# Performance work log

Measured on AMD Instinct MI355X. Metric: run time of the kernel, lower is better.

Reference implementation:

```python
import jax, jax.numpy as jnp
import numpy as np

N = 1024   # state dimension
L = 16384  # sequence length


def setup_inputs() -> dict:
    key = jax.random.key(0)
    k_u, k_a, k_b, k_c = jax.random.split(key, 4)
    u = jax.random.normal(k_u, (L,), dtype=jnp.float32)
    # lecun_normal: std = 1/sqrt(fan_in). Shift A by -I so the discretized
    # transition matrix Ab has spectral radius < 1 (otherwise Ab^L overflows).
    A = jax.random.normal(k_a, (N, N), dtype=jnp.float32) / np.sqrt(N) - jnp.eye(N, dtype=jnp.float32)
    B = jax.random.normal(k_b, (N, 1), dtype=jnp.float32) / np.sqrt(1.0)
    C = jax.random.normal(k_c, (1, N), dtype=jnp.float32) / np.sqrt(N)
    log_step = jnp.full((1, 1), np.log(0.01), dtype=jnp.float32)
    return {"u": u, "A": A, "B": B, "C": C, "log_step": log_step}


def reference(u, A, B, C, log_step):
    # --- discretize (bilinear / Tustin transform) ---
    step = jnp.exp(log_step)[0, 0]
    I = jnp.eye(A.shape[0], dtype=A.dtype)
    BL = jnp.linalg.inv(I - (step / 2.0) * A)
    Ab = BL @ (I + (step / 2.0) * A)     # (N, N)
    Bb = (step * BL) @ B                  # (N, 1)
    Cb = C                                # (1, N)

    # --- naive_kernel: K[l] = Cb @ Ab^l @ Bb, built as a scan recurrence ---
    def body(x, _):
        k_l = (Cb @ x)[0, 0]
        return Ab @ x, k_l

    _, K = jax.lax.scan(body, Bb, None, length=u.shape[0])  # (L,)

    # --- causal convolution: y[t] = sum_{l<=t} K[l] * u[t-l] ---
    y = jnp.convolve(u, K)[: u.shape[0]]
    return y
```

## Files before the change

### kernel.cpp

```cpp
#include <hip/hip_runtime.h>
#include <hip/hip_bf16.h>
#include <math.h>

#define N_DIM 1024
#define L_SEQ 16384

typedef unsigned short ushort_t;
typedef __bf16 bf16x8 __attribute__((ext_vector_type(8)));
typedef float f32x4 __attribute__((ext_vector_type(4)));

#define FW_F32 1
#define FW_SPLIT 2
#define FW_TSPLIT 4
#define FW_ADDD 8
#define FW_MKAB 16
#define FW_TPRE 32

#define AS1 __attribute__((address_space(1)))
#define AS3 __attribute__((address_space(3)))

__device__ __forceinline__ void split2(float v, ushort_t& h, ushort_t& m) {
  union { __bf16 b; ushort_t u; } c;
  __bf16 bh = (__bf16)v;
  float fh = (float)bh;
  c.b = bh; h = c.u;
  c.b = (__bf16)(v - fh); m = c.u;
}

__global__ __launch_bounds__(256) void k_scalesplit(const float* __restrict__ A,
    const float* __restrict__ ls, float* __restrict__ E,
    ushort_t* __restrict__ set) {
  const size_t NN = (size_t)N_DIM * N_DIM;
  float hs = 0.5f * expf(ls[0]);
  int t = threadIdx.x;
  int r0 = blockIdx.x * 64 + ((t >> 4) << 2);
  int c0 = blockIdx.y * 64 + ((t & 15) << 2);
  float v[4][4];
#pragma unroll
  for (int i = 0; i < 4; ++i) {
    float4 f = *(const float4*)&A[(size_t)(r0 + i) * N_DIM + c0];
    v[i][0] = hs * f.x; v[i][1] = hs * f.y; v[i][2] = hs * f.z; v[i][3] = hs * f.w;
    *(float4*)&E[(size_t)(r0 + i) * N_DIM + c0] =
        make_float4(v[i][0], v[i][1], v[i][2], v[i][3]);
  }
  ushort_t h[4][4], m[4][4];
#pragma unroll
  for (int i = 0; i < 4; ++i)
#pragma unroll
    for (int j = 0; j < 4; ++j) split2(v[i][j], h[i][j], m[i][j]);
#pragma unroll
  for (int i = 0; i < 4; ++i) {
    size_t o = (size_t)(r0 + i) * N_DIM + c0;
    *(ushort4*)&set[o] = make_ushort4(h[i][0], h[i][1], h[i][2], h[i][3]);
    *(ushort4*)&set[NN + o] = make_ushort4(m[i][0], m[i][1], m[i][2], m[i][3]);
  }
#pragma unroll
  for (int j = 0; j < 4; ++j) {
    size_t o = (size_t)(c0 + j) * N_DIM + r0;
    *(ushort4*)&set[2 * NN + o] = make_ushort4(h[0][j], h[1][j], h[2][j], h[3][j]);
    *(ushort4*)&set[3 * NN + o] = make_ushort4(m[0][j], m[1][j], m[2][j], m[3][j]);
  }
}

__global__ __launch_bounds__(256) void k_bbinit(ushort_t* __restrict__ VTset,
    ushort_t* __restrict__ Wset, const float* __restrict__ S,
    const float* __restrict__ B, const float* __restrict__ Cm,
    const float* __restrict__ ls) {
  const size_t KR = (size_t)128 * N_DIM;
  int bx = blockIdx.x;
  if (bx >= 256) {
    int i = (bx - 256) * 256 + threadIdx.x;
    ushort_t h, m; split2(Cm[i], h, m);
    Wset[i] = h; Wset[KR + i] = m;
    return;
  }
  int row = bx * 4 + (threadIdx.x >> 6);
  int lane = threadIdx.x & 63;
  const float* Sr = S + (size_t)row * N_DIM;
  float sum = 0.f;
  for (int k = lane; k < N_DIM; k += 64) sum += Sr[k] * B[k];
  for (int off = 32; off; off >>= 1) sum += __shfl_down(sum, off);
  if (lane == 0) {
    float step = expf(ls[0]);
    float bb = step * (B[row] + sum);
    ushort_t h, m; split2(bb, h, m);
    VTset[row] = h; VTset[KR + row] = m;
  }
}

__global__ __launch_bounds__(256) void gemm4f(
    const ushort_t* __restrict__ Qa, const ushort_t* __restrict__ Qbt,
    const float* __restrict__ D, float* __restrict__ Cf,
    ushort_t* __restrict__ Oset, ushort_t* __restrict__ Oset2, int flags,
    const ushort_t* __restrict__ SkB, ushort_t* __restrict__ Ka,
    int srcOff, int dstOff, int cnt, int mode) {
  const size_t NN = (size_t)N_DIM * N_DIM;
  const size_t KR = (size_t)128 * N_DIM;
  __shared__ __align__(16) ushort_t lds[32768];
  int t = threadIdx.x;
  const int lane = t & 63, w = t >> 6;
  bool isSk = (mode == 2) || (mode == 1 && (int)blockIdx.y >= 16);

  if (!isSk) {
    int m0 = blockIdx.x * 64, n0 = blockIdx.y * 64;
    int r = t & 63, kc = t >> 6;
    const ushort_t* gA[2] = {Qa, Qa + NN};
    const ushort_t* gB[2] = {Qbt, Qbt + NN};
    size_t aoff = (size_t)(m0 + r) * N_DIM + kc * 8;
    size_t boff = (size_t)(n0 + r) * N_DIM + kc * 8;

    auto stage = [&](int buf, int k0) {
      ushort_t* dst = lds + buf * 8192;
#pragma unroll
      for (int L = 0; L < 2; ++L) {
        __builtin_amdgcn_global_load_lds(
            (const AS1 void*)(gA[L] + aoff + k0),
            (AS3 void*)(dst + L * 2048 + t * 8), 16, 0, 0);
        __builtin_amdgcn_global_load_lds(
            (const AS1 void*)(gB[L] + boff + k0),
            (AS3 void*)(dst + 4096 + L * 2048 + t * 8), 16, 0, 0);
      }
    };

    f32x4 acc[2][2];
#pragma unroll
    for (int i = 0; i < 2; ++i)
#pragma unroll
      for (int j = 0; j < 2; ++j) acc[i][j] = (f32x4){0.f, 0.f, 0.f, 0.f};

    const int wm = (w >> 1) * 32, wn = (w & 1) * 32;
    const int lrow = lane & 15, kg = lane >> 4;
    const int aIdx0 = kg * 512 + (wm + lrow) * 8;
    const int bIdx0 = 4096 + kg * 512 + (wn + lrow) * 8;

    stage(0, 0);
    stage(1, 32);
    stage(2, 64);
    for (int ks = 0; ks < 32; ++ks) {
      int cur = ks & 3;
      if (ks < 29) {
        stage((ks + 3) & 3, (ks + 3) * 32);
        asm volatile("s_waitcnt vmcnt(12)" ::: "memory");
      } else if (ks == 29) {
        asm volatile("s_waitcnt vmcnt(8)" ::: "memory");
      } else if (ks == 30) {
        asm volatile("s_waitcnt vmcnt(4)" ::: "memory");
      } else {
        asm volatile("s_waitcnt vmcnt(0)" ::: "memory");
      }
      __builtin_amdgcn_s_barrier();
      __builtin_amdgcn_sched_barrier(0);
      const ushort_t* buf = lds + cur * 8192;
      bf16x8 a[2][2], b[2][2];
#pragma unroll
      for (int L = 0; L < 2; ++L) {
#pragma unroll
        for (int mi = 0; mi < 2; ++mi)
          a[L][mi] = *(const bf16x8*)&buf[L * 2048 + aIdx0 + mi * 128];
#pragma unroll
        for (int ni = 0; ni < 2; ++ni)
          b[L][ni] = *(const bf16x8*)&buf[bIdx0 + L * 2048 + ni * 128];
      }
#pragma unroll
      for (int mi = 0; mi < 2; ++mi)
#pragma unroll
        for (int ni = 0; ni < 2; ++ni) {
          f32x4 c = acc[mi][ni];
          c = __builtin_amdgcn_mfma_f32_16x16x32_bf16(a[0][mi], b[0][ni], c, 0, 0, 0);
          c = __builtin_amdgcn_mfma_f32_16x16x32_bf16(a[0][mi], b[1][ni], c, 0, 0, 0);
          c = __builtin_amdgcn_mfma_f32_16x16x32_bf16(a[1][mi], b[0][ni], c, 0, 0, 0);
          c = __builtin_amdgcn_mfma_f32_16x16x32_bf16(a[1][mi], b[1][ni], c, 0, 0, 0);
          acc[mi][ni] = c;
        }
      if (ks < 31) __builtin_amdgcn_s_barrier();
    }

#pragma unroll
    for (int mi = 0; mi < 2; ++mi)
#pragma unroll
      for (int ni = 0; ni < 2; ++ni) {
        int rowb = m0 + wm + mi * 16 + kg * 4;
        int col = n0 + wn + ni * 16 + lrow;
        float vv[4];
#pragma unroll
        for (int j = 0; j < 4; ++j) vv[j] = acc[mi][ni][j];
        if (flags & FW_TPRE) {
          ushort_t h[4], m[4];
#pragma unroll
          for (int j = 0; j < 4; ++j) split2(vv[j], h[j], m[j]);
          size_t o = (size_t)col * N_DIM + rowb;
          *(ushort4*)&Oset2[2 * NN + o] = make_ushort4(h[0], h[1], h[2], h[3]);
          *(ushort4*)&Oset2[3 * NN + o] = make_ushort4(m[0], m[1], m[2], m[3]);
        }
        if (flags & FW_ADDD) {
#pragma unroll
          for (int j = 0; j < 4; ++j) vv[j] += D[(size_t)(rowb + j) * N_DIM + col];
        }
        if (flags & FW_F32) {
#pragma unroll
          for (int j = 0; j < 4; ++j) Cf[(size_t)(rowb + j) * N_DIM + col] = vv[j];
        }
        if (flags & FW_MKAB) {
#pragma unroll
          for (int j = 0; j < 4; ++j)
            vv[j] = 2.0f * vv[j] + ((rowb + j) == col ? 1.0f : 0.0f);
        }
        if (flags & (FW_SPLIT | FW_TSPLIT)) {
          ushort_t h[4], m[4];
#pragma unroll
          for (int j = 0; j < 4; ++j) split2(vv[j], h[j], m[j]);
          if (flags & FW_SPLIT) {
#pragma unroll
            for (int j = 0; j < 4; ++j) {
              size_t o = (size_t)(rowb + j) * N_DIM + col;
              Oset[o] = h[j]; Oset[NN + o] = m[j];
            }
          }
          if (flags & FW_TSPLIT) {
            size_t o = (size_t)col * N_DIM + rowb;
            *(ushort4*)&Oset[2 * NN + o] = make_ushort4(h[0], h[1], h[2], h[3]);
            *(ushort4*)&Oset[3 * NN + o] = make_ushort4(m[0], m[1], m[2], m[3]);
          }
        }
      }
    return;
  }

  int id = (mode == 1) ? ((int)blockIdx.y - 16) * 16 + (int)blockIdx.x
                       : (int)blockIdx.y * 16 + (int)blockIdx.x;
  int rt = id >> 4, ct = id & 15;
  if (rt >= ((cnt + 15) >> 4)) return;
  const ushort_t* Ah = Ka;
  const ushort_t* Amm = Ka + KR;
  const ushort_t* Bh = SkB;
  const ushort_t* Bm = SkB + NN;
  const int lrow = lane & 15, kg = lane >> 4;

  auto stageS = [&](int buf, int k0) {
    ushort_t* base = lds + buf * 5120;
    if (t < 128) {
      int lvl = t >> 6, rem = t & 63, kcc = rem >> 4, i = rem & 15;
      const ushort_t* src = (lvl ? Amm : Ah) +
          (size_t)(srcOff + rt * 16 + i) * N_DIM + k0 + kcc * 8;
      __builtin_amdgcn_global_load_lds((const AS1 void*)src,
                                       (AS3 void*)(base + t * 8), 16, 0, 0);
    }
#pragma unroll
    for (int it2 = 0; it2 < 2; ++it2) {
      int t2 = t + it2 * 256;
      int lvl = t2 >> 8, rem = t2 & 255, kcc = rem >> 6, c = rem & 63;
      const ushort_t* src =
          (lvl ? Bm : Bh) + (size_t)(ct * 64 + c) * N_DIM + k0 + kcc * 8;
      __builtin_amdgcn_global_load_lds(
          (const AS1 void*)src, (AS3 void*)(base + 1024 + t2 * 8), 16, 0, 0);
    }
  };

  f32x4 acc = (f32x4){0.f, 0.f, 0.f, 0.f};
  const int aO = kg * 128 + lrow * 8;
  const int bO = 1024 + kg * 512 + (w * 16 + lrow) * 8;

  stageS(0, 0);
  stageS(1, 32);
  for (int ks2 = 0; ks2 < 32; ++ks2) {
    int cur = ks2 % 3;
    if (ks2 < 30) {
      stageS((ks2 + 2) % 3, (ks2 + 2) * 32);
      if (w < 2) asm volatile("s_waitcnt vmcnt(6)" ::: "memory");
      else       asm volatile("s_waitcnt vmcnt(4)" ::: "memory");
    } else if (ks2 == 30) {
      if (w < 2) asm volatile("s_waitcnt vmcnt(3)" ::: "memory");
      else       asm volatile("s_waitcnt vmcnt(2)" ::: "memory");
    } else {
      asm volatile("s_waitcnt vmcnt(0)" ::: "memory");
    }
    __builtin_amdgcn_s_barrier();
    __builtin_amdgcn_sched_barrier(0);
    const ushort_t* b = lds + cur * 5120;
    bf16x8 a0 = *(const bf16x8*)&b[aO];
    bf16x8 a1 = *(const bf16x8*)&b[aO + 512];
    bf16x8 b0v = *(const bf16x8*)&b[bO];
    bf16x8 b1v = *(const bf16x8*)&b[bO + 2048];
    acc = __builtin_amdgcn_mfma_f32_16x16x32_bf16(a0, b0v, acc, 0, 0, 0);
    acc = __builtin_amdgcn_mfma_f32_16x16x32_bf16(a0, b1v, acc, 0, 0, 0);
    acc = __builtin_amdgcn_mfma_f32_16x16x32_bf16(a1, b0v, acc, 0, 0, 0);
    acc = __builtin_amdgcn_mfma_f32_16x16x32_bf16(a1, b1v, acc, 0, 0, 0);
    if (ks2 < 31) __builtin_amdgcn_s_barrier();
  }

  int col = ct * 64 + w * 16 + lrow;
#pragma unroll
  for (int j = 0; j < 4; ++j) {
    int ir = rt * 16 + kg * 4 + j;
    if (ir < cnt) {
      ushort_t h, m; split2(acc[j], h, m);
      Ka[(size_t)(dstOff + ir) * N_DIM + col] = h;
      Ka[KR + (size_t)(dstOff + ir) * N_DIM + col] = m;
    }
  }
}

__global__ __launch_bounds__(256) void k_combine(
    const ushort_t* __restrict__ Wset, const ushort_t* __restrict__ Vset,
    float* __restrict__ Kv) {
  const size_t KR = (size_t)128 * N_DIM;
  __shared__ __align__(16) ushort_t lds[15360];
  int t = threadIdx.x;
  int rt = blockIdx.x, ct = blockIdx.y;
  const ushort_t* Ah = Wset;
  const ushort_t* Amm = Wset + KR;
  const ushort_t* Bh = Vset;
  const ushort_t* Bm = Vset + KR;
  const int lane = t & 63, w = t >> 6;
  const int lrow = lane & 15, kg = lane >> 4;

  auto stageS = [&](int buf, int k0) {
    ushort_t* base = lds + buf * 5120;
    if (t < 128) {
      int lvl = t >> 6, rem = t & 63, kcc = rem >> 4, i = rem & 15;
      const ushort_t* src =
          (lvl ? Amm : Ah) + (size_t)(rt * 16 + i) * N_DIM + k0 + kcc * 8;
      __builtin_amdgcn_global_load_lds((const AS1 void*)src,
                                       (AS3 void*)(base + t * 8), 16, 0, 0);
    }
#pragma unroll
    for (int it = 0; it < 2; ++it) {
      int t2 = t + it * 256;
      int lvl = t2 >> 8, rem = t2 & 255, kcc = rem >> 6, c = rem & 63;
      const ushort_t* src =
          (lvl ? Bm : Bh) + (size_t)(ct * 64 + c) * N_DIM + k0 + kcc * 8;
      __builtin_amdgcn_global_load_lds(
          (const AS1 void*)src, (AS3 void*)(base + 1024 + t2 * 8), 16, 0, 0);
    }
  };

  f32x4 acc = (f32x4){0.f, 0.f, 0.f, 0.f};
  const int aO = kg * 128 + lrow * 8;
  const int bO = 1024 + kg * 512 + (w * 16 + lrow) * 8;

  stageS(0, 0);
  stageS(1, 32);
  for (int ks = 0; ks < 32; ++ks) {
    int cur = ks % 3;
    if (ks < 30) {
      stageS((ks + 2) % 3, (ks + 2) * 32);
      if (w < 2) asm volatile("s_waitcnt vmcnt(6)" ::: "memory");
      else       asm volatile("s_waitcnt vmcnt(4)" ::: "memory");
    } else if (ks == 30) {
      if (w < 2) asm volatile("s_waitcnt vmcnt(3)" ::: "memory");
      else       asm volatile("s_waitcnt vmcnt(2)" ::: "memory");
    } else {
      asm volatile("s_waitcnt vmcnt(0)" ::: "memory");
    }
    __builtin_amdgcn_s_barrier();
    __builtin_amdgcn_sched_barrier(0);
    const ushort_t* b = lds + cur * 5120;
    bf16x8 a0 = *(const bf16x8*)&b[aO];
    bf16x8 a1 = *(const bf16x8*)&b[aO + 512];
    bf16x8 b0v = *(const bf16x8*)&b[bO];
    bf16x8 b1v = *(const bf16x8*)&b[bO + 2048];
    acc = __builtin_amdgcn_mfma_f32_16x16x32_bf16(a0, b0v, acc, 0, 0, 0);
    acc = __builtin_amdgcn_mfma_f32_16x16x32_bf16(a0, b1v, acc, 0, 0, 0);
    acc = __builtin_amdgcn_mfma_f32_16x16x32_bf16(a1, b0v, acc, 0, 0, 0);
    acc = __builtin_amdgcn_mfma_f32_16x16x32_bf16(a1, b1v, acc, 0, 0, 0);
    if (ks < 31) __builtin_amdgcn_s_barrier();
  }

  int rcol = ct * 64 + w * 16 + lrow;
#pragma unroll
  for (int j = 0; j < 4; ++j) {
    int q = rt * 16 + kg * 4 + j;
    Kv[q * 128 + rcol] = acc[j];
  }
}

__global__ __launch_bounds__(256) void conv_k(const float* __restrict__ Kv,
    const float* __restrict__ u, float* __restrict__ y) {
  const int CT = 1024, CJ = 256, LCH = 1024;
  int t0 = blockIdx.x * CT;
  int l0 = blockIdx.y * LCH;
  if (l0 > t0 + CT - 1) return;
  __shared__ __align__(16) float Ks[CJ];
  __shared__ __align__(16) float us[CT + CJ + 8];
  int tid = threadIdx.x;
  float acc0 = 0.f, acc1 = 0.f, acc2 = 0.f, acc3 = 0.f;
  int ltEnd = l0 + LCH; if (ltEnd > t0 + CT) ltEnd = t0 + CT;
  for (int lt = l0; lt < ltEnd; lt += CJ) {
    __syncthreads();
    Ks[tid] = Kv[lt + tid];
    int ub = t0 - lt - (CJ - 1);
    for (int s = tid; s < CT + CJ + 4; s += 256) {
      int g = ub + s;
      us[s] = (g >= 0 && g < L_SEQ) ? u[g] : 0.f;
    }
    __syncthreads();
    const float4* u4 = (const float4*)us;
    float4 wa = u4[tid];
#pragma unroll 4
    for (int jb = 0; jb < CJ / 4; ++jb) {
      float4 wb = u4[tid + jb + 1];
      float4 k4 = *(const float4*)&Ks[CJ - 4 - (jb << 2)];
      acc0 += k4.w * wa.x + k4.z * wa.y + k4.y * wa.z + k4.x * wa.w;
      acc1 += k4.w * wa.y + k4.z * wa.z + k4.y * wa.w + k4.x * wb.x;
      acc2 += k4.w * wa.z + k4.z * wa.w + k4.y * wb.x + k4.x * wb.y;
      acc3 += k4.w * wa.w + k4.z * wb.x + k4.y * wb.y + k4.x * wb.z;
      wa = wb;
    }
  }
  int t = t0 + (tid << 2);
  atomicAdd(&y[t + 0], acc0);
  atomicAdd(&y[t + 1], acc1);
  atomicAdd(&y[t + 2], acc2);
  atomicAdd(&y[t + 3], acc3);
}


extern "C" void kernel_launch(void* const* d_in, const int* in_sizes, int n_in,
                              void* d_out, int out_size, void* d_ws, size_t ws_size,
                              hipStream_t stream) {
  const float* u  = (const float*)d_in[0];
  const float* A  = (const float*)d_in[1];
  const float* B  = (const float*)d_in[2];
  const float* Cm = (const float*)d_in[3];
  const float* ls = (const float*)d_in[4];
  float* y  = (float*)d_out;
  float* ws = (float*)d_ws;

  const int N = N_DIM;
  const size_t NN = (size_t)N * N;
  const size_t KR = (size_t)128 * N;
  float* b0 = ws;
  float* b2 = b0 + NN;
  float* Kv = b2 + NN;
  ushort_t* setA = (ushort_t*)(Kv + L_SEQ);
  ushort_t* setB = setA + 4 * NN;
  ushort_t* setC = setB + 4 * NN;
  ushort_t* VTset = setC + 4 * NN;
  ushort_t* Wset = VTset + 2 * KR;

  hipMemsetAsync(y, 0, (size_t)L_SEQ * sizeof(float), stream);

  dim3 g16(16, 16);
  dim3 gFull(16, 20);
  dim3 gSk32(16, 2);

  k_scalesplit<<<g16, 256, 0, stream>>>(A, ls, b0, setA);
  gemm4f<<<g16, 256, 0, stream>>>(setA, setA + 2 * NN, b0, b2, setC, setB,
                                  FW_TPRE | FW_ADDD | FW_F32 | FW_SPLIT,
                                  nullptr, nullptr, 0, 0, 0, 0);
  gemm4f<<<g16, 256, 0, stream>>>(setC, setB + 2 * NN, b2, b0, setA, nullptr,
                                  FW_ADDD | FW_F32 | FW_MKAB | FW_SPLIT | FW_TSPLIT,
                                  nullptr, nullptr, 0, 0, 0, 0);
  k_bbinit<<<260, 256, 0, stream>>>(VTset, Wset, b0, B, Cm, ls);

  ushort_t* cur = setA;
  ushort_t* oth = setB;
  for (int e = 0; e < 12; ++e) {
    int right = (e < 7);
    int s = 1 << (right ? e : (e - 7));
    ushort_t* Ka = right ? VTset : Wset;
    const ushort_t* SkB = right ? cur : cur + 2 * NN;
    int fl = (e == 11) ? FW_TSPLIT : (FW_SPLIT | FW_TSPLIT);
    gemm4f<<<gFull, 256, 0, stream>>>(cur, cur + 2 * NN, nullptr, nullptr,
                                      oth, nullptr, fl, SkB, Ka, 0, s, s, 1);
    ushort_t* tmp = cur; cur = oth; oth = tmp;
  }
  const ushort_t* Q12T = cur + 2 * NN;
  for (int p = 0; p < 3; ++p)
    gemm4f<<<gSk32, 256, 0, stream>>>(cur, cur, nullptr, nullptr,
                                      nullptr, nullptr, 0, Q12T, Wset,
                                      32 * p, 32 + 32 * p, 32, 2);
  k_combine<<<dim3(8, 2), 256, 0, stream>>>(Wset, VTset, Kv);
  conv_k<<<g16, 256, 0, stream>>>(Kv, u, y);
}
```

Baseline: 475.2 us.

## Fold skinny GEMM into square-tile blocks and narrow skinny tiles

The skinny (vector-block) product used to run in extra grid rows (16x20 grid) alongside the square GEMM. Now every block of a 16x16 grid runs its square tile and then a 16x16 skinny tile after a sync. Skinny tiles shrink from 16x64 to 16x16 with only one wave doing MFMA, and the standalone skinny launches use 16x8 grids. This removes the extra blocks per squaring launch. In exchange the skinny work is serialized after the GEMM tile inside each block, and three of four waves sit idle during it.

```diff
diff --git a/kernel.cpp b/kernel.cpp
--- a/kernel.cpp
+++ b/kernel.cpp
@@ -88,6 +88,82 @@
   }
 }
 
+__device__ __forceinline__ void skinny_q(
+    ushort_t* lds, const ushort_t* __restrict__ SkB, ushort_t* __restrict__ Ka,
+    int srcOff, int dstOff, int cnt, int id, int t) {
+  const size_t NN = (size_t)N_DIM * N_DIM;
+  const size_t KR = (size_t)128 * N_DIM;
+  int rt = id >> 6, c16 = id & 63;
+  if (rt * 16 >= cnt) return;
+  const int lane = t & 63, w = t >> 6;
+  const ushort_t* Ah = Ka;
+  const ushort_t* Amm = Ka + KR;
+  const ushort_t* Bh = SkB;
+  const ushort_t* Bm = SkB + NN;
+
+  auto stq = [&](int buf, int k0) {
+    ushort_t* base = lds + buf * 2048;
+    if (t < 128) {
+      int pl = t >> 6, rem = t & 63, kc = rem >> 4, row = rem & 15;
+      const ushort_t* src = (pl ? Amm : Ah) +
+          (size_t)(srcOff + rt * 16 + row) * N_DIM + k0 + kc * 8;
+      __builtin_amdgcn_global_load_lds((const AS1 void*)src,
+                                       (AS3 void*)(base + t * 8), 16, 0, 0);
+    } else {
+      int t2 = t - 128;
+      int pl = t2 >> 6, rem = t2 & 63, kc = rem >> 4, row = rem & 15;
+      const ushort_t* src = (pl ? Bm : Bh) +
+          (size_t)(c16 * 16 + row) * N_DIM + k0 + kc * 8;
+      __builtin_amdgcn_global_load_lds((const AS1 void*)src,
+                                       (AS3 void*)(base + 1024 + t2 * 8), 16, 0, 0);
+    }
+  };
+
+  f32x4 acc = (f32x4){0.f, 0.f, 0.f, 0.f};
+  const int lrow = lane & 15, kg = lane >> 4;
+
+  stq(0, 0);
+  stq(1, 32);
+  for (int ks = 0; ks < 32; ++ks) {
+    int cur = ks % 3;
+    if (ks < 30) {
+      stq((ks + 2) % 3, (ks + 2) * 32);
+      asm volatile("s_waitcnt vmcnt(2)" ::: "memory");
+    } else if (ks == 30) {
+      asm volatile("s_waitcnt vmcnt(1)" ::: "memory");
+    } else {
+      asm volatile("s_waitcnt vmcnt(0)" ::: "memory");
+    }
+    __builtin_amdgcn_s_barrier();
+    __builtin_amdgcn_sched_barrier(0);
+    if (w == 0) {
+      const ushort_t* b = lds + cur * 2048;
+      bf16x8 a0 = *(const bf16x8*)&b[kg * 128 + lrow * 8];
+      bf16x8 a1 = *(const bf16x8*)&b[512 + kg * 128 + lrow * 8];
+      bf16x8 b0 = *(const bf16x8*)&b[1024 + kg * 128 + lrow * 8];
+      bf16x8 b1 = *(const bf16x8*)&b[1536 + kg * 128 + lrow * 8];
+      acc = __builtin_amdgcn_mfma_f32_16x16x32_bf16(a0, b0, acc, 0, 0, 0);
+      acc = __builtin_amdgcn_mfma_f32_16x16x32_bf16(a0, b1, acc, 0, 0, 0);
+      acc = __builtin_amdgcn_mfma_f32_16x16x32_bf16(a1, b0, acc, 0, 0, 0);
+      acc = __builtin_amdgcn_mfma_f32_16x16x32_bf16(a1, b1, acc, 0, 0, 0);
+    }
+    if (ks < 31) __builtin_amdgcn_s_barrier();
+  }
+
+  if (w == 0) {
+    int col = c16 * 16 + lrow;
+#pragma unroll
+    for (int j = 0; j < 4; ++j) {
+      int irl = kg * 4 + j;
+      if (rt * 16 + irl < cnt) {
+        ushort_t h, m; split2(acc[j], h, m);
+        Ka[(size_t)(dstOff + rt * 16 + irl) * N_DIM + col] = h;
+        Ka[KR + (size_t)(dstOff + rt * 16 + irl) * N_DIM + col] = m;
+      }
+    }
+  }
+}
+
 __global__ __launch_bounds__(256) void gemm4f(
     const ushort_t* __restrict__ Qa, const ushort_t* __restrict__ Qbt,
     const float* __restrict__ D, float* __restrict__ Cf,
@@ -95,13 +171,17 @@
     const ushort_t* __restrict__ SkB, ushort_t* __restrict__ Ka,
     int srcOff, int dstOff, int cnt, int mode) {
   const size_t NN = (size_t)N_DIM * N_DIM;
-  const size_t KR = (size_t)128 * N_DIM;
   __shared__ __align__(16) ushort_t lds[32768];
   int t = threadIdx.x;
   const int lane = t & 63, w = t >> 6;
-  bool isSk = (mode == 2) || (mode == 1 && (int)blockIdx.y >= 16);
-
-  if (!isSk) {
+  int id = (int)blockIdx.y * 16 + (int)blockIdx.x;
+
+  if (mode == 2) {
+    skinny_q(lds, SkB, Ka, srcOff, dstOff, cnt, id, t);
+    return;
+  }
+
+  {
     int m0 = blockIdx.x * 64, n0 = blockIdx.y * 64;
     int r = t & 63, kc = t >> 6;
     const ushort_t* gA[2] = {Qa, Qa + NN};
@@ -223,80 +303,11 @@
           }
         }
       }
-    return;
-  }
-
-  int id = (mode == 1) ? ((int)blockIdx.y - 16) * 16 + (int)blockIdx.x
-                       : (int)blockIdx.y * 16 + (int)blockIdx.x;
-  int rt = id >> 4, ct = id & 15;
-  if (rt >= ((cnt + 15) >> 4)) return;
-  const ushort_t* Ah = Ka;
-  const ushort_t* Amm = Ka + KR;
-  const ushort_t* Bh = SkB;
-  const ushort_t* Bm = SkB + NN;
-  const int lrow = lane & 15, kg = lane >> 4;
-
-  auto stageS = [&](int buf, int k0) {
-    ushort_t* base = lds + buf * 5120;
-    if (t < 128) {
-      int lvl = t >> 6, rem = t & 63, kcc = rem >> 4, i = rem & 15;
-      const ushort_t* src = (lvl ? Amm : Ah) +
-          (size_t)(srcOff + rt * 16 + i) * N_DIM + k0 + kcc * 8;
-      __builtin_amdgcn_global_load_lds((const AS1 void*)src,
-                                       (AS3 void*)(base + t * 8), 16, 0, 0);
-    }
-#pragma unroll
-    for (int it2 = 0; it2 < 2; ++it2) {
-      int t2 = t + it2 * 256;
-      int lvl = t2 >> 8, rem = t2 & 255, kcc = rem >> 6, c = rem & 63;
-      const ushort_t* src =
-          (lvl ? Bm : Bh) + (size_t)(ct * 64 + c) * N_DIM + k0 + kcc * 8;
-      __builtin_amdgcn_global_load_lds(
-          (const AS1 void*)src, (AS3 void*)(base + 1024 + t2 * 8), 16, 0, 0);
-    }
-  };
-
-  f32x4 acc = (f32x4){0.f, 0.f, 0.f, 0.f};
-  const int aO = kg * 128 + lrow * 8;
-  const int bO = 1024 + kg * 512 + (w * 16 + lrow) * 8;
-
-  stageS(0, 0);
-  stageS(1, 32);
-  for (int ks2 = 0; ks2 < 32; ++ks2) {
-    int cur = ks2 % 3;
-    if (ks2 < 30) {
-      stageS((ks2 + 2) % 3, (ks2 + 2) * 32);
-      if (w < 2) asm volatile("s_waitcnt vmcnt(6)" ::: "memory");
-      else       asm volatile("s_waitcnt vmcnt(4)" ::: "memory");
-    } else if (ks2 == 30) {
-      if (w < 2) asm volatile("s_waitcnt vmcnt(3)" ::: "memory");
-      else       asm volatile("s_waitcnt vmcnt(2)" ::: "memory");
-    } else {
-      asm volatile("s_waitcnt vmcnt(0)" ::: "memory");
-    }
-    __builtin_amdgcn_s_barrier();
-    __builtin_amdgcn_sched_barrier(0);
-    const ushort_t* b = lds + cur * 5120;
-    bf16x8 a0 = *(const bf16x8*)&b[aO];
-    bf16x8 a1 = *(const bf16x8*)&b[aO + 512];
-    bf16x8 b0v = *(const bf16x8*)&b[bO];
-    bf16x8 b1v = *(const bf16x8*)&b[bO + 2048];
-    acc = __builtin_amdgcn_mfma_f32_16x16x32_bf16(a0, b0v, acc, 0, 0, 0);
-    acc = __builtin_amdgcn_mfma_f32_16x16x32_bf16(a0, b1v, acc, 0, 0, 0);
-    acc = __builtin_amdgcn_mfma_f32_16x16x32_bf16(a1, b0v, acc, 0, 0, 0);
-    acc = __builtin_amdgcn_mfma_f32_16x16x32_bf16(a1, b1v, acc, 0, 0, 0);
-    if (ks2 < 31) __builtin_amdgcn_s_barrier();
-  }
-
-  int col = ct * 64 + w * 16 + lrow;
-#pragma unroll
-  for (int j = 0; j < 4; ++j) {
-    int ir = rt * 16 + kg * 4 + j;
-    if (ir < cnt) {
-      ushort_t h, m; split2(acc[j], h, m);
-      Ka[(size_t)(dstOff + ir) * N_DIM + col] = h;
-      Ka[KR + (size_t)(dstOff + ir) * N_DIM + col] = m;
-    }
+  }
+
+  if (mode == 1) {
+    __syncthreads();
+    skinny_q(lds, SkB, Ka, srcOff, dstOff, cnt, id, t);
   }
 }
 
@@ -441,8 +452,7 @@
   hipMemsetAsync(y, 0, (size_t)L_SEQ * sizeof(float), stream);
 
   dim3 g16(16, 16);
-  dim3 gFull(16, 20);
-  dim3 gSk32(16, 2);
+  dim3 gQ32(16, 8);
 
   k_scalesplit<<<g16, 256, 0, stream>>>(A, ls, b0, setA);
   gemm4f<<<g16, 256, 0, stream>>>(setA, setA + 2 * NN, b0, b2, setC, setB,
@@ -461,15 +471,15 @@
     ushort_t* Ka = right ? VTset : Wset;
     const ushort_t* SkB = right ? cur : cur + 2 * NN;
     int fl = (e == 11) ? FW_TSPLIT : (FW_SPLIT | FW_TSPLIT);
-    gemm4f<<<gFull, 256, 0, stream>>>(cur, cur + 2 * NN, nullptr, nullptr,
-                                      oth, nullptr, fl, SkB, Ka, 0, s, s, 1);
+    gemm4f<<<g16, 256, 0, stream>>>(cur, cur + 2 * NN, nullptr, nullptr,
+                                    oth, nullptr, fl, SkB, Ka, 0, s, s, 1);
     ushort_t* tmp = cur; cur = oth; oth = tmp;
   }
   const ushort_t* Q12T = cur + 2 * NN;
   for (int p = 0; p < 3; ++p)
-    gemm4f<<<gSk32, 256, 0, stream>>>(cur, cur, nullptr, nullptr,
-                                      nullptr, nullptr, 0, Q12T, Wset,
-                                      32 * p, 32 + 32 * p, 32, 2);
+    gemm4f<<<gQ32, 256, 0, stream>>>(cur, cur, nullptr, nullptr,
+                                     nullptr, nullptr, 0, Q12T, Wset,
+                                     32 * p, 32 + 32 * p, 32, 2);
   k_combine<<<dim3(8, 2), 256, 0, stream>>>(Wset, VTset, Kv);
   conv_k<<<g16, 256, 0, stream>>>(Kv, u, y);
 }
```

Measured after the change: 414.1 us. -12.9%, faster.
